# Optimization experiments

Measured on AMD Instinct MI355X. Metric: run time of the kernel, lower is better.

The kernel has to match this reference:

```python
import jax, jax.numpy as jnp
import numpy as np

B, N, D = 4, 2048, 1024
HEAD_DIMS = 128
NUM_HEADS = 8
PROJ = HEAD_DIMS * NUM_HEADS  # 1024


def setup_inputs() -> dict:
    key = jax.random.key(0)
    ks = jax.random.split(key, 5)
    # Weights stored as (in, out); xavier-normal-like scale
    def xavier(k, fan_in, fan_out):
        std = (2.0 / (fan_in + fan_out)) ** 0.5
        return jax.random.normal(k, (fan_in, fan_out), dtype=jnp.float32) * std
    return {
        "x": jax.random.normal(ks[0], (B, N, D), dtype=jnp.float32),
        "Wq": xavier(ks[1], D, PROJ),
        "Wk": xavier(ks[2], D, PROJ),
        "Wv": xavier(ks[3], D, PROJ),
        "Wo": xavier(ks[4], PROJ, PROJ),
    }


def reference(x, Wq, Wk, Wv, Wo):
    b, n, d = x.shape
    # QKV projections, split into heads: (b, h, n, hd)
    def split_heads(z):
        return z.reshape(b, n, NUM_HEADS, HEAD_DIMS).transpose(0, 2, 1, 3)
    q = split_heads(x @ Wq)
    k = split_heads(x @ Wk)
    v = split_heads(x @ Wv)
    scale = 1.0 / jnp.sqrt(jnp.float32(HEAD_DIMS))
    logits = jnp.einsum("bhqd,bhkd->bhqk", q, k) * scale
    weights = jax.nn.softmax(logits, axis=-1)
    out = jnp.einsum("bhqk,bhkd->bhqd", weights, v)
    out = out.transpose(0, 2, 1, 3).reshape(b, n, PROJ)
    return out @ Wo
```

## Files before the change

kernel.cpp:

```cpp
#include <hip/hip_runtime.h>
#include <hip/hip_bf16.h>


typedef __attribute__((ext_vector_type(8))) short short8;
typedef __attribute__((ext_vector_type(4))) short short4v;
typedef __attribute__((ext_vector_type(4))) float floatx4;
typedef __attribute__((ext_vector_type(8))) _Float16 half8;

#define MFMA_F16(a, b, c) __builtin_amdgcn_mfma_f32_16x16x32_f16( \
    __builtin_bit_cast(half8, (a)), __builtin_bit_cast(half8, (b)), (c), 0, 0, 0)

static constexpr int BATCH  = 4;
static constexpr int NHEADS = 8;
static constexpr int SEQ    = 2048;
static constexpr int HD     = 128;
static constexpr int DMODEL = 1024;
static constexpr int MROWS  = BATCH * SEQ;
static constexpr int NQKV   = 3 * DMODEL;

#define QSCALE2 0.12752283786512624f

static __device__ __forceinline__ short f16bits(float v) {
    return __builtin_bit_cast(short, (_Float16)v);
}

template <typename T>
static __device__ __forceinline__ short8 load8_f16(const T* p) {
    if constexpr (sizeof(T) == 2) {
        return *(const short8*)p;
    } else {
        const float4 f0 = *(const float4*)p;
        const float4 f1 = *(const float4*)(p + 4);
        short8 r;
        r[0] = f16bits(f0.x); r[1] = f16bits(f0.y);
        r[2] = f16bits(f0.z); r[3] = f16bits(f0.w);
        r[4] = f16bits(f1.x); r[5] = f16bits(f1.y);
        r[6] = f16bits(f1.z); r[7] = f16bits(f1.w);
        return r;
    }
}

static __device__ __forceinline__ void storeC(float* C, size_t idx, float v) {
    C[idx] = v;
}
static __device__ __forceinline__ void storeC(_Float16* C, size_t idx, float v) {
    C[idx] = (_Float16)v;
}

static __device__ __forceinline__ void gload16(const short* g, short* l) {
    __builtin_amdgcn_global_load_lds(
        (const __attribute__((address_space(1))) void*)g,
        (__attribute__((address_space(3))) void*)l, 16, 0, 0);
}

__global__ __launch_bounds__(256)
void prep(const float* __restrict__ x, short* __restrict__ xb,
          const float* __restrict__ W0, const float* __restrict__ W1,
          const float* __restrict__ W2, const float* __restrict__ W3,
          short* __restrict__ Wt, int K, int N)
{
    __shared__ short T[32][33];
    const int z = blockIdx.z;
    if (z >= 4) {
        const size_t chunk = ((size_t)(z - 4) * 1024 + blockIdx.y * 32 + blockIdx.x);
        const size_t i = (chunk * 256 + threadIdx.x) * 8;
        *(short8*)&xb[i] = load8_f16(&x[i]);
        return;
    }
    const float* W = (z == 0) ? W0 : (z == 1) ? W1 : (z == 2) ? W2 : W3;
    short* Wtz = Wt + (size_t)z * K * N;

    const int n0 = blockIdx.x * 32, k0 = blockIdx.y * 32;
    const int r = threadIdx.x >> 3, c4 = (threadIdx.x & 7) * 4;

    const float4 v = *(const float4*)&W[(size_t)(k0 + r) * N + n0 + c4];
    T[r][c4 + 0] = f16bits(v.x);
    T[r][c4 + 1] = f16bits(v.y);
    T[r][c4 + 2] = f16bits(v.z);
    T[r][c4 + 3] = f16bits(v.w);
    __syncthreads();

    short4v o;
    o[0] = T[c4 + 0][r]; o[1] = T[c4 + 1][r];
    o[2] = T[c4 + 2][r]; o[3] = T[c4 + 3][r];
    *(short4v*)&Wtz[(size_t)(n0 + r) * K + k0 + c4] = o;
}

__global__ __launch_bounds__(256)
void convx(const float* __restrict__ x, short* __restrict__ xb)
{
    const size_t i = ((size_t)blockIdx.x * 256 + threadIdx.x) * 8;
    *(short8*)&xb[i] = load8_f16(&x[i]);
}

template <typename OutT, bool QKV>
__global__ __launch_bounds__(256)
void gemm128(const short* __restrict__ A, const short* __restrict__ Bt,
             OutT* __restrict__ C, int M, int N, int K, size_t qkvStride)
{
    __shared__ __align__(16) short As[128 * 64];
    __shared__ __align__(16) short Bs[128 * 64];

    const int tid  = threadIdx.x;
    const int lane = tid & 63;
    const int w    = tid >> 6;
    const int quad = lane >> 4;
    const int l16  = lane & 15;

    const int m0 = blockIdx.x * 128;
    const int n0 = blockIdx.y * 128;
    const int wm = (w >> 1) * 64;
    const int wn = (w & 1) * 64;

    floatx4 acc[4][4] = {};

    const int srow   = tid >> 3;
    const int schunk = (tid & 7) ^ (srow & 7);
    const short* aG = A  + (size_t)(m0 + srow) * K + schunk * 8;
    const short* bG = Bt + (size_t)(n0 + srow) * K + schunk * 8;
    short* aL = As + tid * 8;
    short* bL = Bs + tid * 8;

    const int fsw = l16 & 7;

    for (int k0 = 0; k0 < K; k0 += 64) {
        __syncthreads();
        #pragma unroll
        for (int r = 0; r < 4; ++r) {
            gload16(aG + k0 + (size_t)(r * 32) * K, aL + r * 2048);
            gload16(bG + k0 + (size_t)(r * 32) * K, bL + r * 2048);
        }
        __syncthreads();

        #pragma unroll
        for (int kk = 0; kk < 2; ++kk) {
            short8 af[4], bf[4];
            #pragma unroll
            for (int mi = 0; mi < 4; ++mi)
                af[mi] = *(short8*)&As[(wm + mi * 16 + l16) * 64 +
                                       (((kk * 4 + quad) ^ fsw) * 8)];
            #pragma unroll
            for (int ni = 0; ni < 4; ++ni)
                bf[ni] = *(short8*)&Bs[(wn + ni * 16 + l16) * 64 +
                                       (((kk * 4 + quad) ^ fsw) * 8)];

            #pragma unroll
            for (int mi = 0; mi < 4; ++mi)
                #pragma unroll
                for (int ni = 0; ni < 4; ++ni)
                    acc[mi][ni] = MFMA_F16(af[mi], bf[ni], acc[mi][ni]);
        }
    }

    #pragma unroll
    for (int mi = 0; mi < 4; ++mi)
        #pragma unroll
        for (int ni = 0; ni < 4; ++ni) {
            if constexpr (QKV) {
                const int n   = n0 + wn + ni * 16 + l16;
                const int qkv = n >> 10, rem = n & 1023;
                const int hh  = rem >> 7, d = rem & 127;
                const int mb  = m0 + wm + mi * 16 + quad * 4;
                const int bb  = mb >> 11, s = mb & 2047;
                if (qkv == 2) {
                    short4v pk;
                    #pragma unroll
                    for (int r = 0; r < 4; ++r)
                        pk[r] = f16bits(acc[mi][ni][r]);
                    *(short4v*)&((short*)C)[2 * qkvStride +
                        (((size_t)bb * NHEADS + hh) * HD + d) * SEQ + s] = pk;
                } else {
                    const float sc = (qkv == 0) ? QSCALE2 : 1.0f;
                    #pragma unroll
                    for (int r = 0; r < 4; ++r)
                        storeC(C, (size_t)qkv * qkvStride +
                                  (((size_t)bb * NHEADS + hh) * SEQ + s + r) * HD + d,
                               acc[mi][ni][r] * sc);
                }
            } else {
                #pragma unroll
                for (int r = 0; r < 4; ++r) {
                    const int m = m0 + wm + mi * 16 + quad * 4 + r;
                    const int n = n0 + wn + ni * 16 + l16;
                    storeC(C, (size_t)m * N + n, acc[mi][ni][r]);
                }
            }
        }
}

__global__ __launch_bounds__(256)
void attn_flash10(const short* __restrict__ Q, const short* __restrict__ K,
                  const short* __restrict__ Vt, _Float16* __restrict__ O)
{
    __shared__ __align__(16) short Ks[2][32 * 128];
    __shared__ __align__(16) short Vs[2][128 * 32];
    __shared__ __align__(16) short Plds[4][16 * 40];

    const int tid  = threadIdx.x;
    const int lane = tid & 63;
    const int w    = tid >> 6;
    const int quad = lane >> 4;
    const int l16  = lane & 15;

    const int h  = blockIdx.x & 7;
    const int qi = blockIdx.x >> 3;
    const int b  = blockIdx.y;
    const int q0 = qi * 64;

    const short* Qh  = Q  + (((size_t)b * NHEADS + h) * SEQ) * HD;
    const short* Kh  = K  + (((size_t)b * NHEADS + h) * SEQ) * HD;
    const short* Vth = Vt + (((size_t)b * NHEADS + h) * HD) * SEQ;

    const int qrow = q0 + w * 16 + l16;
    short8 qf[4];
    #pragma unroll
    for (int c = 0; c < 4; ++c)
        qf[c] = *(const short8*)&Qh[(size_t)qrow * HD + c * 32 + quad * 8];

    const int kr0 = tid >> 4, kc0 = tid & 15;
    const int kr1 = kr0 + 16;
    const short* kGa = Kh + (size_t)kr0 * HD + ((kc0 ^ (kr0 & 15)) * 8);
    const short* kGb = Kh + (size_t)kr1 * HD + ((kc0 ^ (kr1 & 15)) * 8);
    const int vr0 = tid >> 2, vp0 = tid & 3;
    const short* vGa = Vth + (size_t)vr0 * SEQ + ((vp0 ^ ((vr0 >> 1) & 3)) * 8);
    const short* vGb = Vth + (size_t)(vr0 + 64) * SEQ + ((vp0 ^ ((vr0 >> 1) & 3)) * 8);

    floatx4 acc[8] = {};
    floatx4 acc9 = {};

    short8 ones;
    #pragma unroll
    for (int j = 0; j < 8; ++j) ones[j] = 0x3C00;

    const int fswV = (l16 >> 1) & 3;
    short* Pw = &Plds[w][0];

    auto STAGE = [&](short* kDst, short* vDst, int tile) {
        const size_t ko = (size_t)tile * 32 * HD;
        const size_t vo = (size_t)tile * 32;
        gload16(kGa + ko, kDst + tid * 8);
        gload16(kGb + ko, kDst + (tid + 256) * 8);
        gload16(vGa + vo, vDst + tid * 8);
        gload16(vGb + vo, vDst + (tid + 256) * 8);
    };

    auto COMPUTE = [&](const short* Kb, const short* Vb) {
        floatx4 s0 = {}, s1 = {};
        __builtin_amdgcn_s_setprio(1);
        #pragma unroll
        for (int c = 0; c < 4; ++c) {
            const int k_ = c * 4 + quad;
            short8 kf0 = *(short8*)&Kb[l16 * 128 + ((k_ ^ l16) * 8)];
            short8 kf1 = *(short8*)&Kb[(16 + l16) * 128 + ((k_ ^ l16) * 8)];
            s0 = MFMA_F16(qf[c], kf0, s0);
            s1 = MFMA_F16(qf[c], kf1, s1);
        }
        __builtin_amdgcn_s_setprio(0);
        #pragma unroll
        for (int r = 0; r < 4; ++r) {
            const float p0 = __builtin_amdgcn_exp2f(s0[r]);
            const float p1 = __builtin_amdgcn_exp2f(s1[r]);
            Pw[(quad * 4 + r) * 40 + l16]      = f16bits(p0);
            Pw[(quad * 4 + r) * 40 + 16 + l16] = f16bits(p1);
        }
        short8 pf = *(short8*)&Pw[l16 * 40 + quad * 8];
        __builtin_amdgcn_s_setprio(1);
        acc9 = MFMA_F16(pf, ones, acc9);
        #pragma unroll
        for (int hc = 0; hc < 8; ++hc) {
            short8 vf = *(short8*)&Vb[(hc * 16 + l16) * 32 + ((quad ^ fswV) * 8)];
            acc[hc] = MFMA_F16(pf, vf, acc[hc]);
        }
        __builtin_amdgcn_s_setprio(0);
    };

    STAGE(&Ks[0][0], &Vs[0][0], 0);

    for (int kt = 0; kt < SEQ; kt += 64) {
        const int t = kt >> 5;
        __syncthreads();
        STAGE(&Ks[1][0], &Vs[1][0], t + 1);
        COMPUTE(&Ks[0][0], &Vs[0][0]);
        __syncthreads();
        if (kt + 64 < SEQ)
            STAGE(&Ks[0][0], &Vs[0][0], t + 2);
        COMPUTE(&Ks[1][0], &Vs[1][0]);
    }

    float rinv[4];
    #pragma unroll
    for (int r = 0; r < 4; ++r)
        rinv[r] = 1.0f / fmaxf(acc9[r], 1e-30f);

    #pragma unroll
    for (int hc = 0; hc < 8; ++hc)
        #pragma unroll
        for (int r = 0; r < 4; ++r) {
            const int row = q0 + w * 16 + quad * 4 + r;
            O[((size_t)b * SEQ + row) * DMODEL + h * HD + hc * 16 + l16] =
                (_Float16)(acc[hc][r] * rinv[r]);
        }
}

template <typename AT, typename OutT>
__global__ __launch_bounds__(256)
void gemm64(const AT* __restrict__ A, const float* __restrict__ W,
            OutT* __restrict__ C, int M, int N, int K, int headsplit)
{
    __shared__ __align__(16) short As[64][32];
    __shared__ __align__(16) short Bs[64][32];

    const int tid  = threadIdx.x;
    const int lane = tid & 63;
    const int w    = tid >> 6;
    const int quad = lane >> 4;
    const int l16  = lane & 15;

    const int m0 = blockIdx.x * 64;
    const int n0 = blockIdx.y * 64;
    const int wm = (w >> 1) * 32;
    const int wn = (w & 1) * 32;

    floatx4 acc[2][2] = {};

    const int arow = tid >> 2, acol = (tid & 3) * 8;
    const int brow = tid >> 3, bcol = (tid & 7) * 8;

    const AT*    aptr = A + (size_t)(m0 + arow) * K + acol;
    const float* bptr = W + (size_t)brow * N + n0 + bcol;

    for (int k0 = 0; k0 < K; k0 += 32) {
        short8 av = load8_f16(aptr + k0);
        short8 bv = load8_f16(bptr + (size_t)k0 * N);
        __syncthreads();
        *(short8*)&As[arow][acol] = av;
        #pragma unroll
        for (int j = 0; j < 8; ++j)
            Bs[bcol + j][brow] = bv[j];
        __syncthreads();

        short8 af0 = *(short8*)&As[wm + l16][quad * 8];
        short8 af1 = *(short8*)&As[wm + 16 + l16][quad * 8];
        short8 bf0 = *(short8*)&Bs[wn + l16][quad * 8];
        short8 bf1 = *(short8*)&Bs[wn + 16 + l16][quad * 8];

        acc[0][0] = MFMA_F16(af0, bf0, acc[0][0]);
        acc[0][1] = MFMA_F16(af0, bf1, acc[0][1]);
        acc[1][0] = MFMA_F16(af1, bf0, acc[1][0]);
        acc[1][1] = MFMA_F16(af1, bf1, acc[1][1]);
    }

    #pragma unroll
    for (int mi = 0; mi < 2; ++mi)
        #pragma unroll
        for (int ni = 0; ni < 2; ++ni)
            #pragma unroll
            for (int r = 0; r < 4; ++r) {
                const int m = m0 + wm + mi * 16 + quad * 4 + r;
                const int n = n0 + wn + ni * 16 + l16;
                const float v = acc[mi][ni][r];
                if (headsplit) {
                    const int b = m >> 11, nn = m & 2047;
                    const int h = n >> 7,  d  = n & 127;
                    storeC(C, (((size_t)b * NHEADS + h) * SEQ + nn) * HD + d, v);
                } else {
                    storeC(C, (size_t)m * N + n, v);
                }
            }
}

__global__ __launch_bounds__(256)
void attn_flash(const short* __restrict__ Q, const short* __restrict__ K,
                const short* __restrict__ V, _Float16* __restrict__ O)
{
    __shared__ __align__(16) short Ksf[32][136];
    __shared__ __align__(16) short Vtl[HD][40];
    __shared__ __align__(16) short Pldsf[4][16][40];

    const int tid  = threadIdx.x;
    const int lane = tid & 63;
    const int w    = tid >> 6;
    const int quad = lane >> 4;
    const int l16  = lane & 15;

    const int q0 = blockIdx.x * 64;
    const int h  = blockIdx.y;
    const int b  = blockIdx.z;

    const size_t headoff = ((size_t)b * NHEADS + h) * SEQ * HD;
    const short* Qh = Q + headoff;
    const short* Kh = K + headoff;
    const short* Vh = V + headoff;

    const float scale = 0.08838834764831845f;

    const int qrow = q0 + w * 16 + l16;
    short8 qf[4];
    #pragma unroll
    for (int c = 0; c < 4; ++c)
        qf[c] = *(const short8*)&Qh[(size_t)qrow * HD + c * 32 + quad * 8];

    float mrow[4], lrow[4];
    #pragma unroll
    for (int r = 0; r < 4; ++r) { mrow[r] = -1e30f; lrow[r] = 0.f; }
    floatx4 acc[8] = {};

    const int krow = tid >> 4, kcol = (tid & 15) * 8;
    const int vkey = tid & 31;
    const int vhd  = (tid >> 5) * 16;

    for (int kt = 0; kt < SEQ; kt += 32) {
        const short* Kt = Kh + (size_t)kt * HD;
        short8 k0v = *(const short8*)(Kt + (size_t)tid * 8);
        short8 k1v = *(const short8*)(Kt + (size_t)(tid + 256) * 8);
        short8 v0 = *(const short8*)&Vh[(size_t)(kt + vkey) * HD + vhd];
        short8 v1 = *(const short8*)&Vh[(size_t)(kt + vkey) * HD + vhd + 8];

        __syncthreads();
        *(short8*)&Ksf[krow][kcol]      = k0v;
        *(short8*)&Ksf[krow + 16][kcol] = k1v;
        #pragma unroll
        for (int j = 0; j < 8; ++j) {
            Vtl[vhd + j][vkey]     = v0[j];
            Vtl[vhd + 8 + j][vkey] = v1[j];
        }
        __syncthreads();

        floatx4 s0 = {}, s1 = {};
        #pragma unroll
        for (int c = 0; c < 4; ++c) {
            short8 kf0 = *(short8*)&Ksf[l16][c * 32 + quad * 8];
            short8 kf1 = *(short8*)&Ksf[16 + l16][c * 32 + quad * 8];
            s0 = MFMA_F16(qf[c], kf0, s0);
            s1 = MFMA_F16(qf[c], kf1, s1);
        }

        float p0[4], p1[4], alpha[4];
        #pragma unroll
        for (int r = 0; r < 4; ++r) {
            const float a  = s0[r] * scale;
            const float bb = s1[r] * scale;
            float mx = fmaxf(a, bb);
            mx = fmaxf(mx, __shfl_xor(mx, 1));
            mx = fmaxf(mx, __shfl_xor(mx, 2));
            mx = fmaxf(mx, __shfl_xor(mx, 4));
            mx = fmaxf(mx, __shfl_xor(mx, 8));
            const float mnew = fmaxf(mrow[r], mx);
            alpha[r] = __expf(mrow[r] - mnew);
            mrow[r]  = mnew;
            p0[r] = __expf(a - mnew);
            p1[r] = __expf(bb - mnew);
            float rs = p0[r] + p1[r];
            rs += __shfl_xor(rs, 1);
            rs += __shfl_xor(rs, 2);
            rs += __shfl_xor(rs, 4);
            rs += __shfl_xor(rs, 8);
            lrow[r] = lrow[r] * alpha[r] + rs;
        }
        #pragma unroll
        for (int hc = 0; hc < 8; ++hc)
            #pragma unroll
            for (int r = 0; r < 4; ++r)
                acc[hc][r] *= alpha[r];

        #pragma unroll
        for (int r = 0; r < 4; ++r) {
            Pldsf[w][quad * 4 + r][l16]      = f16bits(p0[r]);
            Pldsf[w][quad * 4 + r][16 + l16] = f16bits(p1[r]);
        }
        __syncthreads();

        short8 pf = *(short8*)&Pldsf[w][l16][quad * 8];
        #pragma unroll
        for (int hc = 0; hc < 8; ++hc) {
            short8 vf = *(short8*)&Vtl[hc * 16 + l16][quad * 8];
            acc[hc] = MFMA_F16(pf, vf, acc[hc]);
        }
    }

    #pragma unroll
    for (int hc = 0; hc < 8; ++hc)
        #pragma unroll
        for (int r = 0; r < 4; ++r) {
            const int row = q0 + w * 16 + quad * 4 + r;
            const float val = acc[hc][r] / fmaxf(lrow[r], 1e-30f);
            O[((size_t)b * SEQ + row) * DMODEL + h * HD + hc * 16 + l16] =
                (_Float16)val;
        }
}

extern "C" void kernel_launch(void* const* d_in, const int* in_sizes, int n_in,
                              void* d_out, int out_size, void* d_ws, size_t ws_size,
                              hipStream_t stream)
{
    const float* x  = (const float*)d_in[0];
    const float* Wq = (const float*)d_in[1];
    const float* Wk = (const float*)d_in[2];
    const float* Wv = (const float*)d_in[3];
    const float* Wo = (const float*)d_in[4];
    float* out = (float*)d_out;

    const size_t bufElems = (size_t)MROWS * DMODEL;
    const size_t batElems = (size_t)SEQ * DMODEL;
    const size_t MiB = 1024 * 1024;
    dim3 tt(256);

    if (ws_size >= 72 * MiB) {
        short* xb    = (short*)d_ws;
        short* Qb    = xb + bufElems;
        short* Kb    = xb + 2 * bufElems;
        short* Vtb   = xb + 3 * bufElems;
        short* Wtall = xb + 4 * bufElems;
        short* Wto   = Wtall + 3 * (size_t)DMODEL * DMODEL;
        short* Ab    = xb;

        prep<<<dim3(32, 32, 8), tt, 0, stream>>>(
            x, xb, Wq, Wk, Wv, Wo, Wtall, DMODEL, DMODEL);

        gemm128<_Float16, true><<<dim3(MROWS / 128, NQKV / 128), tt, 0, stream>>>(
            xb, Wtall, (_Float16*)Qb, MROWS, NQKV, DMODEL, bufElems);

        attn_flash10<<<dim3(NHEADS * (SEQ / 64), BATCH), tt, 0, stream>>>(
            Qb, Kb, Vtb, (_Float16*)Ab);

        gemm128<float, false><<<dim3(MROWS / 128, DMODEL / 128), tt, 0, stream>>>(
            Ab, Wto, out, MROWS, DMODEL, DMODEL, 0);
    } else if (ws_size >= 64 * MiB) {
        short* xb    = (short*)d_ws;
        short* Qb    = xb + 2 * batElems;
        short* Kb    = Qb + 4 * batElems;
        short* Vtb   = Kb + 4 * batElems;
        short* Wtall = Vtb + 4 * batElems;
        short* Wto   = Wtall + 3 * (size_t)DMODEL * DMODEL;

        prep<<<dim3(32, 32, 4), tt, 0, stream>>>(
            nullptr, nullptr, Wq, Wk, Wv, Wo, Wtall, DMODEL, DMODEL);

        for (int half = 0; half < 2; ++half) {
            const size_t off = (size_t)half * 2 * batElems;
            convx<<<dim3(2048), tt, 0, stream>>>(x + off, xb);
            gemm128<_Float16, true><<<dim3(32, NQKV / 128), tt, 0, stream>>>(
                xb, Wtall, (_Float16*)(Qb + off), 2 * SEQ, NQKV, DMODEL,
                4 * batElems);
        }
        for (int half = 0; half < 2; ++half) {
            const size_t off = (size_t)half * 2 * batElems;
            attn_flash10<<<dim3(NHEADS * (SEQ / 64), 2), tt, 0, stream>>>(
                Qb + off, Kb + off, Vtb + off, (_Float16*)xb);
            gemm128<float, false><<<dim3(32, DMODEL / 128), tt, 0, stream>>>(
                xb, Wto, out + off, 2 * SEQ, DMODEL, DMODEL, 0);
        }
    } else if (ws_size >= 24 * MiB) {
        short* xb    = (short*)d_ws;
        short* Qb    = xb + batElems;
        short* Kb    = xb + 2 * batElems;
        short* Vtb   = xb + 3 * batElems;
        short* Wtall = xb + 4 * batElems;
        short* Wto   = Wtall + 3 * (size_t)DMODEL * DMODEL;

        prep<<<dim3(32, 32, 4), tt, 0, stream>>>(
            nullptr, nullptr, Wq, Wk, Wv, Wo, Wtall, DMODEL, DMODEL);

        for (int b = 0; b < BATCH; ++b) {
            convx<<<dim3(1024), tt, 0, stream>>>(x + (size_t)b * batElems, xb);
            gemm128<_Float16, true><<<dim3(SEQ / 128, NQKV / 128), tt, 0, stream>>>(
                xb, Wtall, (_Float16*)Qb, SEQ, NQKV, DMODEL, batElems);
            attn_flash10<<<dim3(NHEADS * (SEQ / 64), 1), tt, 0, stream>>>(
                Qb, Kb, Vtb, (_Float16*)xb);
            gemm128<float, false><<<dim3(SEQ / 128, DMODEL / 128), tt, 0, stream>>>(
                xb, Wto, out + (size_t)b * batElems, SEQ, DMODEL, DMODEL, 0);
        }
    } else {
        short* Qb = (short*)d_ws;
        short* Kb = Qb + batElems;
        short* Vb = Qb + 2 * batElems;
        short* Ab = Qb + 3 * batElems;

        dim3 gg(SEQ / 64, DMODEL / 64);
        for (int b = 0; b < BATCH; ++b) {
            const float* xb_ = x + (size_t)b * batElems;
            gemm64<float, _Float16><<<gg, tt, 0, stream>>>(
                xb_, Wq, (_Float16*)Qb, SEQ, DMODEL, DMODEL, 1);
            gemm64<float, _Float16><<<gg, tt, 0, stream>>>(
                xb_, Wk, (_Float16*)Kb, SEQ, DMODEL, DMODEL, 1);
            gemm64<float, _Float16><<<gg, tt, 0, stream>>>(
                xb_, Wv, (_Float16*)Vb, SEQ, DMODEL, DMODEL, 1);
            attn_flash<<<dim3(SEQ / 64, NHEADS, 1), tt, 0, stream>>>(
                Qb, Kb, Vb, (_Float16*)Ab);
            gemm64<short, float><<<gg, tt, 0, stream>>>(
                Ab, Wo, out + (size_t)b * batElems, SEQ, DMODEL, DMODEL, 0);
        }
    }
}
```

Measured before the change: 275.6 us.

## Split attention KV range across warp pairs with 32-row query tiles per warp

Each warp now handles 32 query rows, and the four warps are split into two query halves and two KV halves. Every K/V fragment read from LDS therefore feeds two MFMAs, and the partial accumulators are merged through shared memory at the end. The double-buffered prefetch pipeline is dropped in favour of a load, sync, compute sequence over two KV tiles at a time. This raises register pressure and exposes global-load latency, in exchange for halving LDS reads per MFMA.

New measurement: 289.3 us. 5.0% more time.

```diff
diff --git a/kernel.cpp b/kernel.cpp
--- a/kernel.cpp
+++ b/kernel.cpp
@@ -189,18 +189,18 @@
 }
 
 __global__ __launch_bounds__(256)
-void attn_flash10(const short* __restrict__ Q, const short* __restrict__ K,
+void attn_flash14(const short* __restrict__ Q, const short* __restrict__ K,
                   const short* __restrict__ Vt, _Float16* __restrict__ O)
 {
-    __shared__ __align__(16) short Ks[2][32 * 128];
-    __shared__ __align__(16) short Vs[2][128 * 32];
-    __shared__ __align__(16) short Plds[4][16 * 40];
+    __shared__ __align__(16) short POOL[21504];
 
     const int tid  = threadIdx.x;
     const int lane = tid & 63;
     const int w    = tid >> 6;
     const int quad = lane >> 4;
     const int l16  = lane & 15;
+    const int qhalf = w & 1;
+    const int khalf = w >> 1;
 
     const int h  = blockIdx.x & 7;
     const int qi = blockIdx.x >> 3;
@@ -211,11 +211,14 @@
     const short* Kh  = K  + (((size_t)b * NHEADS + h) * SEQ) * HD;
     const short* Vth = Vt + (((size_t)b * NHEADS + h) * HD) * SEQ;
 
-    const int qrow = q0 + w * 16 + l16;
-    short8 qf[4];
+    short8 qf[2][4];
     #pragma unroll
-    for (int c = 0; c < 4; ++c)
-        qf[c] = *(const short8*)&Qh[(size_t)qrow * HD + c * 32 + quad * 8];
+    for (int mi = 0; mi < 2; ++mi) {
+        const int qrow = q0 + qhalf * 32 + mi * 16 + l16;
+        #pragma unroll
+        for (int c = 0; c < 4; ++c)
+            qf[mi][c] = *(const short8*)&Qh[(size_t)qrow * HD + c * 32 + quad * 8];
+    }
 
     const int kr0 = tid >> 4, kc0 = tid & 15;
     const int kr1 = kr0 + 16;
@@ -225,81 +228,124 @@
     const short* vGa = Vth + (size_t)vr0 * SEQ + ((vp0 ^ ((vr0 >> 1) & 3)) * 8);
     const short* vGb = Vth + (size_t)(vr0 + 64) * SEQ + ((vp0 ^ ((vr0 >> 1) & 3)) * 8);
 
-    floatx4 acc[8] = {};
-    floatx4 acc9 = {};
+    floatx4 acc[2][8] = {};
+    floatx4 acc9[2] = {};
 
     short8 ones;
     #pragma unroll
     for (int j = 0; j < 8; ++j) ones[j] = 0x3C00;
 
     const int fswV = (l16 >> 1) & 3;
-    short* Pw = &Plds[w][0];
-
-    auto STAGE = [&](short* kDst, short* vDst, int tile) {
-        const size_t ko = (size_t)tile * 32 * HD;
-        const size_t vo = (size_t)tile * 32;
-        gload16(kGa + ko, kDst + tid * 8);
-        gload16(kGb + ko, kDst + (tid + 256) * 8);
-        gload16(vGa + vo, vDst + tid * 8);
-        gload16(vGb + vo, vDst + (tid + 256) * 8);
-    };
-
-    auto COMPUTE = [&](const short* Kb, const short* Vb) {
-        floatx4 s0 = {}, s1 = {};
+    short* Pw = POOL + 16384 + w * 1280;
+    const short* Kb = POOL + khalf * 4096;
+    const short* Vb = POOL + 8192 + khalf * 4096;
+
+    for (int t = 0; t < SEQ / 64; ++t) {
+        __syncthreads();
+        #pragma unroll
+        for (int p = 0; p < 2; ++p) {
+            const int g = p * 32 + t;
+            const size_t ko = (size_t)g * 32 * HD;
+            const size_t vo = (size_t)g * 32;
+            short* kDst = POOL + p * 4096;
+            short* vDst = POOL + 8192 + p * 4096;
+            gload16(kGa + ko, kDst + tid * 8);
+            gload16(kGb + ko, kDst + (tid + 256) * 8);
+            gload16(vGa + vo, vDst + tid * 8);
+            gload16(vGb + vo, vDst + (tid + 256) * 8);
+        }
+        __syncthreads();
+
+        floatx4 s[2][2] = {};
         __builtin_amdgcn_s_setprio(1);
         #pragma unroll
         for (int c = 0; c < 4; ++c) {
             const int k_ = c * 4 + quad;
             short8 kf0 = *(short8*)&Kb[l16 * 128 + ((k_ ^ l16) * 8)];
             short8 kf1 = *(short8*)&Kb[(16 + l16) * 128 + ((k_ ^ l16) * 8)];
-            s0 = MFMA_F16(qf[c], kf0, s0);
-            s1 = MFMA_F16(qf[c], kf1, s1);
+            #pragma unroll
+            for (int mi = 0; mi < 2; ++mi) {
+                s[mi][0] = MFMA_F16(qf[mi][c], kf0, s[mi][0]);
+                s[mi][1] = MFMA_F16(qf[mi][c], kf1, s[mi][1]);
+            }
         }
         __builtin_amdgcn_s_setprio(0);
-        #pragma unroll
-        for (int r = 0; r < 4; ++r) {
-            const float p0 = __builtin_amdgcn_exp2f(s0[r]);
-            const float p1 = __builtin_amdgcn_exp2f(s1[r]);
-            Pw[(quad * 4 + r) * 40 + l16]      = f16bits(p0);
-            Pw[(quad * 4 + r) * 40 + 16 + l16] = f16bits(p1);
-        }
-        short8 pf = *(short8*)&Pw[l16 * 40 + quad * 8];
+
+        #pragma unroll
+        for (int mi = 0; mi < 2; ++mi)
+            #pragma unroll
+            for (int r = 0; r < 4; ++r) {
+                const float p0 = __builtin_amdgcn_exp2f(s[mi][0][r]);
+                const float p1 = __builtin_amdgcn_exp2f(s[mi][1][r]);
+                const int prow = mi * 16 + quad * 4 + r;
+                Pw[prow * 40 + l16]      = f16bits(p0);
+                Pw[prow * 40 + 16 + l16] = f16bits(p1);
+            }
+        short8 pf[2];
+        #pragma unroll
+        for (int mi = 0; mi < 2; ++mi)
+            pf[mi] = *(short8*)&Pw[(mi * 16 + l16) * 40 + quad * 8];
+
         __builtin_amdgcn_s_setprio(1);
-        acc9 = MFMA_F16(pf, ones, acc9);
+        #pragma unroll
+        for (int mi = 0; mi < 2; ++mi)
+            acc9[mi] = MFMA_F16(pf[mi], ones, acc9[mi]);
         #pragma unroll
         for (int hc = 0; hc < 8; ++hc) {
             short8 vf = *(short8*)&Vb[(hc * 16 + l16) * 32 + ((quad ^ fswV) * 8)];
-            acc[hc] = MFMA_F16(pf, vf, acc[hc]);
+            #pragma unroll
+            for (int mi = 0; mi < 2; ++mi)
+                acc[mi][hc] = MFMA_F16(pf[mi], vf, acc[mi][hc]);
         }
         __builtin_amdgcn_s_setprio(0);
-    };
-
-    STAGE(&Ks[0][0], &Vs[0][0], 0);
-
-    for (int kt = 0; kt < SEQ; kt += 64) {
-        const int t = kt >> 5;
-        __syncthreads();
-        STAGE(&Ks[1][0], &Vs[1][0], t + 1);
-        COMPUTE(&Ks[0][0], &Vs[0][0]);
-        __syncthreads();
-        if (kt + 64 < SEQ)
-            STAGE(&Ks[0][0], &Vs[0][0], t + 2);
-        COMPUTE(&Ks[1][0], &Vs[1][0]);
-    }
-
-    float rinv[4];
-    #pragma unroll
-    for (int r = 0; r < 4; ++r)
-        rinv[r] = 1.0f / fmaxf(acc9[r], 1e-30f);
-
-    #pragma unroll
-    for (int hc = 0; hc < 8; ++hc)
-        #pragma unroll
-        for (int r = 0; r < 4; ++r) {
-            const int row = q0 + w * 16 + quad * 4 + r;
-            O[((size_t)b * SEQ + row) * DMODEL + h * HD + hc * 16 + l16] =
-                (_Float16)(acc[hc][r] * rinv[r]);
-        }
+    }
+
+    __syncthreads();
+    float* SP = (float*)POOL;
+    if (khalf == 1) {
+        float* dst = SP + (size_t)(qhalf * 64 + lane) * 73;
+        #pragma unroll
+        for (int mi = 0; mi < 2; ++mi) {
+            #pragma unroll
+            for (int hc = 0; hc < 8; ++hc)
+                #pragma unroll
+                for (int r = 0; r < 4; ++r)
+                    dst[mi * 32 + hc * 4 + r] = acc[mi][hc][r];
+            #pragma unroll
+            for (int r = 0; r < 4; ++r)
+                dst[64 + mi * 4 + r] = acc9[mi][r];
+        }
+    }
+    __syncthreads();
+    if (khalf == 0) {
+        const float* src = SP + (size_t)(qhalf * 64 + lane) * 73;
+        #pragma unroll
+        for (int mi = 0; mi < 2; ++mi) {
+            #pragma unroll
+            for (int hc = 0; hc < 8; ++hc)
+                #pragma unroll
+                for (int r = 0; r < 4; ++r)
+                    acc[mi][hc][r] += src[mi * 32 + hc * 4 + r];
+            #pragma unroll
+            for (int r = 0; r < 4; ++r)
+                acc9[mi][r] += src[64 + mi * 4 + r];
+        }
+        #pragma unroll
+        for (int mi = 0; mi < 2; ++mi) {
+            float rinv[4];
+            #pragma unroll
+            for (int r = 0; r < 4; ++r)
+                rinv[r] = 1.0f / fmaxf(acc9[mi][r], 1e-30f);
+            #pragma unroll
+            for (int hc = 0; hc < 8; ++hc)
+                #pragma unroll
+                for (int r = 0; r < 4; ++r) {
+                    const int row = q0 + qhalf * 32 + mi * 16 + quad * 4 + r;
+                    O[((size_t)b * SEQ + row) * DMODEL + h * HD + hc * 16 + l16] =
+                        (_Float16)(acc[mi][hc][r] * rinv[r]);
+                }
+        }
+    }
 }
 
 template <typename AT, typename OutT>
@@ -520,7 +566,7 @@
         gemm128<_Float16, true><<<dim3(MROWS / 128, NQKV / 128), tt, 0, stream>>>(
             xb, Wtall, (_Float16*)Qb, MROWS, NQKV, DMODEL, bufElems);
 
-        attn_flash10<<<dim3(NHEADS * (SEQ / 64), BATCH), tt, 0, stream>>>(
+        attn_flash14<<<dim3(NHEADS * (SEQ / 64), BATCH), tt, 0, stream>>>(
             Qb, Kb, Vtb, (_Float16*)Ab);
 
         gemm128<float, false><<<dim3(MROWS / 128, DMODEL / 128), tt, 0, stream>>>(
@@ -545,7 +591,7 @@
         }
         for (int half = 0; half < 2; ++half) {
             const size_t off = (size_t)half * 2 * batElems;
-            attn_flash10<<<dim3(NHEADS * (SEQ / 64), 2), tt, 0, stream>>>(
+            attn_flash14<<<dim3(NHEADS * (SEQ / 64), 2), tt, 0, stream>>>(
                 Qb + off, Kb + off, Vtb + off, (_Float16*)xb);
             gemm128<float, false><<<dim3(32, DMODEL / 128), tt, 0, stream>>>(
                 xb, Wto, out + off, 2 * SEQ, DMODEL, DMODEL, 0);
@@ -565,7 +611,7 @@
             convx<<<dim3(1024), tt, 0, stream>>>(x + (size_t)b * batElems, xb);
             gemm128<_Float16, true><<<dim3(SEQ / 128, NQKV / 128), tt, 0, stream>>>(
                 xb, Wtall, (_Float16*)Qb, SEQ, NQKV, DMODEL, batElems);
-            attn_flash10<<<dim3(NHEADS * (SEQ / 64), 1), tt, 0, stream>>>(
+            attn_flash14<<<dim3(NHEADS * (SEQ / 64), 1), tt, 0, stream>>>(
                 Qb, Kb, Vtb, (_Float16*)xb);
             gemm128<float, false><<<dim3(SEQ / 128, DMODEL / 128), tt, 0, stream>>>(
                 xb, Wto, out + (size_t)b * batElems, SEQ, DMODEL, DMODEL, 0);
```

## Replace double-buffered K/V staging with single buffer in attention kernel

Applied to the files above, without the earlier changes.

Removes the two-stage K/V LDS ping-pong in the flash attention kernel. Each 32-key tile is now loaded into a single LDS buffer between two barriers, then computed. This halves K/V shared memory, which may raise occupancy, but global loads no longer overlap with MFMA compute within a block. Latency hiding then depends on other resident blocks.

Measured after the change: 279.9 us. Within noise of the previous version (+1.6%).

```diff
diff --git a/kernel.cpp b/kernel.cpp
--- a/kernel.cpp
+++ b/kernel.cpp
@@ -189,11 +189,11 @@
 }
 
 __global__ __launch_bounds__(256)
-void attn_flash10(const short* __restrict__ Q, const short* __restrict__ K,
+void attn_flash15(const short* __restrict__ Q, const short* __restrict__ K,
                   const short* __restrict__ Vt, _Float16* __restrict__ O)
 {
-    __shared__ __align__(16) short Ks[2][32 * 128];
-    __shared__ __align__(16) short Vs[2][128 * 32];
+    __shared__ __align__(16) short Ks[32 * 128];
+    __shared__ __align__(16) short Vs[128 * 32];
     __shared__ __align__(16) short Plds[4][16 * 40];
 
     const int tid  = threadIdx.x;
@@ -235,23 +235,23 @@
     const int fswV = (l16 >> 1) & 3;
     short* Pw = &Plds[w][0];
 
-    auto STAGE = [&](short* kDst, short* vDst, int tile) {
-        const size_t ko = (size_t)tile * 32 * HD;
-        const size_t vo = (size_t)tile * 32;
-        gload16(kGa + ko, kDst + tid * 8);
-        gload16(kGb + ko, kDst + (tid + 256) * 8);
-        gload16(vGa + vo, vDst + tid * 8);
-        gload16(vGb + vo, vDst + (tid + 256) * 8);
-    };
-
-    auto COMPUTE = [&](const short* Kb, const short* Vb) {
+    for (int t = 0; t < SEQ / 32; ++t) {
+        __syncthreads();
+        const size_t ko = (size_t)t * 32 * HD;
+        const size_t vo = (size_t)t * 32;
+        gload16(kGa + ko, Ks + tid * 8);
+        gload16(kGb + ko, Ks + (tid + 256) * 8);
+        gload16(vGa + vo, Vs + tid * 8);
+        gload16(vGb + vo, Vs + (tid + 256) * 8);
+        __syncthreads();
+
         floatx4 s0 = {}, s1 = {};
         __builtin_amdgcn_s_setprio(1);
         #pragma unroll
         for (int c = 0; c < 4; ++c) {
             const int k_ = c * 4 + quad;
-            short8 kf0 = *(short8*)&Kb[l16 * 128 + ((k_ ^ l16) * 8)];
-            short8 kf1 = *(short8*)&Kb[(16 + l16) * 128 + ((k_ ^ l16) * 8)];
+            short8 kf0 = *(short8*)&Ks[l16 * 128 + ((k_ ^ l16) * 8)];
+            short8 kf1 = *(short8*)&Ks[(16 + l16) * 128 + ((k_ ^ l16) * 8)];
             s0 = MFMA_F16(qf[c], kf0, s0);
             s1 = MFMA_F16(qf[c], kf1, s1);
         }
@@ -268,23 +268,10 @@
         acc9 = MFMA_F16(pf, ones, acc9);
         #pragma unroll
         for (int hc = 0; hc < 8; ++hc) {
-            short8 vf = *(short8*)&Vb[(hc * 16 + l16) * 32 + ((quad ^ fswV) * 8)];
+            short8 vf = *(short8*)&Vs[(hc * 16 + l16) * 32 + ((quad ^ fswV) * 8)];
             acc[hc] = MFMA_F16(pf, vf, acc[hc]);
         }
         __builtin_amdgcn_s_setprio(0);
-    };
-
-    STAGE(&Ks[0][0], &Vs[0][0], 0);
-
-    for (int kt = 0; kt < SEQ; kt += 64) {
-        const int t = kt >> 5;
-        __syncthreads();
-        STAGE(&Ks[1][0], &Vs[1][0], t + 1);
-        COMPUTE(&Ks[0][0], &Vs[0][0]);
-        __syncthreads();
-        if (kt + 64 < SEQ)
-            STAGE(&Ks[0][0], &Vs[0][0], t + 2);
-        COMPUTE(&Ks[1][0], &Vs[1][0]);
     }
 
     float rinv[4];
@@ -520,7 +507,7 @@
         gemm128<_Float16, true><<<dim3(MROWS / 128, NQKV / 128), tt, 0, stream>>>(
             xb, Wtall, (_Float16*)Qb, MROWS, NQKV, DMODEL, bufElems);
 
-        attn_flash10<<<dim3(NHEADS * (SEQ / 64), BATCH), tt, 0, stream>>>(
+        attn_flash15<<<dim3(NHEADS * (SEQ / 64), BATCH), tt, 0, stream>>>(
             Qb, Kb, Vtb, (_Float16*)Ab);
 
         gemm128<float, false><<<dim3(MROWS / 128, DMODEL / 128), tt, 0, stream>>>(
@@ -545,7 +532,7 @@
         }
         for (int half = 0; half < 2; ++half) {
             const size_t off = (size_t)half * 2 * batElems;
-            attn_flash10<<<dim3(NHEADS * (SEQ / 64), 2), tt, 0, stream>>>(
+            attn_flash15<<<dim3(NHEADS * (SEQ / 64), 2), tt, 0, stream>>>(
                 Qb + off, Kb + off, Vtb + off, (_Float16*)xb);
             gemm128<float, false><<<dim3(32, DMODEL / 128), tt, 0, stream>>>(
                 xb, Wto, out + off, 2 * SEQ, DMODEL, DMODEL, 0);
@@ -565,7 +552,7 @@
             convx<<<dim3(1024), tt, 0, stream>>>(x + (size_t)b * batElems, xb);
             gemm128<_Float16, true><<<dim3(SEQ / 128, NQKV / 128), tt, 0, stream>>>(
                 xb, Wtall, (_Float16*)Qb, SEQ, NQKV, DMODEL, batElems);
-            attn_flash10<<<dim3(NHEADS * (SEQ / 64), 1), tt, 0, stream>>>(
+            attn_flash15<<<dim3(NHEADS * (SEQ / 64), 1), tt, 0, stream>>>(
                 Qb, Kb, Vtb, (_Float16*)xb);
             gemm128<float, false><<<dim3(SEQ / 128, DMODEL / 128), tt, 0, stream>>>(
                 xb, Wto, out + (size_t)b * batElems, SEQ, DMODEL, DMODEL, 0);
```
